# Kernel tuning notes

Measured on AMD Instinct MI355X. Metric: run time of the kernel, lower is better.

Reference implementation:

```python
import jax, jax.numpy as jnp
import numpy as np

B, S, DIM, H, DH = 1, 4096, 2048, 16, 128
EPS = 1e-5


def setup_inputs() -> dict:
    key = jax.random.key(0)
    ks = jax.random.split(key, 16)
    sc = 0.02
    inp = {
        'hidden_states': jax.random.normal(ks[0], (B, S, DIM), jnp.float32),
        'freqs_cos': jax.random.uniform(ks[1], (1, S, 1, DH), jnp.float32),
        'freqs_sin': jax.random.uniform(ks[2], (1, S, 1, DH), jnp.float32),
        'Wq': jax.random.normal(ks[3], (DIM, DIM), jnp.float32) * sc,
        'bq': jax.random.normal(ks[4], (DIM,), jnp.float32) * sc,
        'Wk': jax.random.normal(ks[5], (DIM, DIM), jnp.float32) * sc,
        'bk': jax.random.normal(ks[6], (DIM,), jnp.float32) * sc,
        'Wv': jax.random.normal(ks[7], (DIM, DIM), jnp.float32) * sc,
        'bv': jax.random.normal(ks[8], (DIM,), jnp.float32) * sc,
        'Wo': jax.random.normal(ks[9], (DIM, DIM), jnp.float32) * sc,
        'bo': jax.random.normal(ks[10], (DIM,), jnp.float32) * sc,
        'gq': jnp.ones((DIM,), jnp.float32),
        'gk': jnp.ones((DIM,), jnp.float32),
    }
    return inp


def _rmsnorm(x, g):
    var = jnp.mean(jnp.square(x), axis=-1, keepdims=True)
    return x * jax.lax.rsqrt(var + EPS) * g


def _apply_rope(x, freqs_cos, freqs_sin):
    # x: [B,S,H,DH]; interleaved rotary as in WanAttnProcessor
    x1 = x[..., 0::2]
    x2 = x[..., 1::2]
    cos = freqs_cos[..., 0::2]
    sin = freqs_sin[..., 1::2]
    o1 = x1 * cos - x2 * sin
    o2 = x1 * sin + x2 * cos
    return jnp.stack([o1, o2], axis=-1).reshape(x.shape)


def reference(hidden_states, freqs_cos, freqs_sin, Wq, bq, Wk, bk, Wv, bv, Wo, bo, gq, gk):
    q = hidden_states @ Wq + bq
    k = hidden_states @ Wk + bk
    v = hidden_states @ Wv + bv
    q = _rmsnorm(q, gq)
    k = _rmsnorm(k, gk)
    q = q.reshape(B, S, H, DH)
    k = k.reshape(B, S, H, DH)
    v = v.reshape(B, S, H, DH)
    q = _apply_rope(q, freqs_cos, freqs_sin)
    k = _apply_rope(k, freqs_cos, freqs_sin)
    scale = 1.0 / np.sqrt(DH).astype(np.float32)
    scores = jnp.einsum('bqhd,bkhd->bhqk', q, k) * scale
    attn = jax.nn.softmax(scores, axis=-1)
    out = jnp.einsum('bhqk,bkhd->bqhd', attn, v)
    out = out.reshape(B, S, H * DH)
    return out @ Wo + bo
```

## Files before the change

kernel.cpp:

```cpp
#include <hip/hip_runtime.h>
#include <hip/hip_bf16.h>

#define SEQ 4096
#define DIMC 2048
#define NH 16
#define DHD 128

typedef short s8v __attribute__((ext_vector_type(8)));
typedef float f4v __attribute__((ext_vector_type(4)));
typedef __bf16 bf8 __attribute__((ext_vector_type(8)));
typedef float f4 __attribute__((ext_vector_type(4)));

typedef __attribute__((address_space(3))) void lds_t;
typedef __attribute__((address_space(1))) void gbl_t;

__device__ __attribute__((aligned(256))) short g_h[(size_t)SEQ * DIMC];
__device__ __attribute__((aligned(256))) short g_q[(size_t)SEQ * DIMC];
__device__ __attribute__((aligned(256))) short g_k[(size_t)SEQ * DIMC];
__device__ __attribute__((aligned(256))) short g_v[(size_t)SEQ * DIMC];
__device__ __attribute__((aligned(256))) short g_vt[(size_t)DIMC * SEQ];
__device__ __attribute__((aligned(256))) short g_wt[4][(size_t)DIMC * DIMC];

__device__ __forceinline__ float b2f(short s) {
    union { unsigned u; float f; } v;
    v.u = ((unsigned)(unsigned short)s) << 16;
    return v.f;
}
__device__ __forceinline__ short f2b(float f) {
    union { float f; unsigned u; } v;
    v.f = f;
    unsigned b = v.u;
    b += 0x7FFFu + ((b >> 16) & 1u);
    return (short)(b >> 16);
}
__device__ __forceinline__ f4 mfma16(bf8 a, bf8 b, f4 c) {
    return __builtin_amdgcn_mfma_f32_16x16x32_bf16(a, b, c, 0, 0, 0);
}
__device__ __forceinline__ void gl_lds16(const short* g, short* l) {
    __builtin_amdgcn_global_load_lds((gbl_t*)g, (lds_t*)l, 16, 0, 0);
}

__global__ __launch_bounds__(256) void conv_h(const float* __restrict__ src) {
    size_t i = ((size_t)blockIdx.x * 256 + threadIdx.x) * 8;
    f4v u0 = *reinterpret_cast<const f4v*>(src + i);
    f4v u1 = *reinterpret_cast<const f4v*>(src + i + 4);
    s8v t;
    for (int j = 0; j < 4; ++j) { t[j] = f2b(u0[j]); t[4 + j] = f2b(u1[j]); }
    *reinterpret_cast<s8v*>(g_h + i) = t;
}

__global__ __launch_bounds__(256) void prep_w(const float* __restrict__ W0,
                                              const float* __restrict__ W1,
                                              const float* __restrict__ W2,
                                              const float* __restrict__ W3) {
    __shared__ __attribute__((aligned(16))) float t[64][68];
    const int z = blockIdx.z;
    const float* W = (z == 0) ? W0 : (z == 1) ? W1 : (z == 2) ? W2 : W3;
    short* WT = g_wt[z];
    const int r0 = blockIdx.y * 64, c0 = blockIdx.x * 64;
    const int tid = threadIdx.x;
    for (int i = 0; i < 4; ++i) {
        int slot = tid + i * 256;
        int r = slot >> 4, c4 = (slot & 15) * 4;
        *reinterpret_cast<f4v*>(&t[r][c4]) =
            *reinterpret_cast<const f4v*>(&W[(size_t)(r0 + r) * DIMC + c0 + c4]);
    }
    __syncthreads();
    for (int i = 0; i < 2; ++i) {
        int slot = tid + i * 256;
        int n = slot >> 3, k8 = (slot & 7) * 8;
        s8v o;
        for (int j = 0; j < 8; ++j) o[j] = f2b(t[k8 + j][n]);
        *reinterpret_cast<s8v*>(&WT[(size_t)(c0 + n) * DIMC + r0 + k8]) = o;
    }
}

template <int DSTF>
__device__ __forceinline__ void gemm_body(const short* __restrict__ X,
                                          const short* __restrict__ Bw,
                                          const float* __restrict__ bias,
                                          short* __restrict__ Yb,
                                          float* __restrict__ Yf,
                                          int bm, int bn) {
    __shared__ __attribute__((aligned(16))) short As[128 * 32];
    __shared__ __attribute__((aligned(16))) short Bs[128 * 32];
    const int tid = threadIdx.x;
    const int w = tid >> 6, lane = tid & 63;
    const int l16 = lane & 15, quad = lane >> 4;
    const int wm = w & 1, wn = w >> 1;

    f4 acc[4][4];
    for (int mi = 0; mi < 4; ++mi)
        for (int ni = 0; ni < 4; ++ni) acc[mi][ni] = (f4)0.0f;

    const int s0 = tid, s1 = tid + 256;
    const int ra0 = s0 >> 2, ca0 = (s0 & 3) * 8;
    const int ra1 = s1 >> 2, ca1 = (s1 & 3) * 8;
    const size_t xo0 = (size_t)(bm * 128 + ra0) * DIMC + ca0;
    const size_t xo1 = (size_t)(bm * 128 + ra1) * DIMC + ca1;
    const size_t bo0 = (size_t)(bn * 128 + ra0) * DIMC + ca0;
    const size_t bo1 = (size_t)(bn * 128 + ra1) * DIMC + ca1;
    short* lda0 = As + (size_t)(0 * 256 + w * 64) * 8;
    short* lda1 = As + (size_t)(1 * 256 + w * 64) * 8;
    short* ldb0 = Bs + (size_t)(0 * 256 + w * 64) * 8;
    short* ldb1 = Bs + (size_t)(1 * 256 + w * 64) * 8;

    for (int kb = 0; kb < DIMC; kb += 32) {
        __syncthreads();
        gl_lds16(X + xo0 + kb, lda0);
        gl_lds16(X + xo1 + kb, lda1);
        gl_lds16(Bw + bo0 + kb, ldb0);
        gl_lds16(Bw + bo1 + kb, ldb1);
        __syncthreads();
        bf8 af[4], bfr[4];
        for (int mi = 0; mi < 4; ++mi)
            af[mi] = *reinterpret_cast<const bf8*>(As + (wm * 64 + mi * 16 + l16) * 32 + quad * 8);
        for (int ni = 0; ni < 4; ++ni)
            bfr[ni] = *reinterpret_cast<const bf8*>(Bs + (wn * 64 + ni * 16 + l16) * 32 + quad * 8);
        for (int mi = 0; mi < 4; ++mi)
            for (int ni = 0; ni < 4; ++ni)
                acc[mi][ni] = mfma16(af[mi], bfr[ni], acc[mi][ni]);
    }

    for (int ni = 0; ni < 4; ++ni) {
        int col = bn * 128 + wn * 64 + ni * 16 + l16;
        float bcol = bias[col];
        for (int mi = 0; mi < 4; ++mi) {
            int row = bm * 128 + wm * 64 + mi * 16 + quad * 4;
            for (int r = 0; r < 4; ++r) {
                if (DSTF)
                    Yf[(size_t)(row + r) * DIMC + col] = acc[mi][ni][r] + bcol;
                else
                    Yb[(size_t)(row + r) * DIMC + col] = f2b(acc[mi][ni][r] + bcol);
            }
        }
    }
}

__global__ __launch_bounds__(256, 2) void gemm_qkv(const float* __restrict__ bq,
                                                   const float* __restrict__ bk,
                                                   const float* __restrict__ bv) {
    const int z = blockIdx.z;
    const float* bias = (z == 0) ? bq : (z == 1) ? bk : bv;
    short* Y = (z == 0) ? g_q : (z == 1) ? g_k : g_v;
    gemm_body<0>(g_h, g_wt[z], bias, Y, nullptr, blockIdx.y, blockIdx.x);
}

__global__ __launch_bounds__(256, 2) void gemm_o(const float* __restrict__ bias,
                                                 float* __restrict__ Yf) {
    gemm_body<1>(g_q, g_wt[3], bias, nullptr, Yf, blockIdx.y, blockIdx.x);
}

__global__ __launch_bounds__(256) void rmsnorm_rope(const float* __restrict__ gq,
                                                    const float* __restrict__ gk,
                                                    const float* __restrict__ fc,
                                                    const float* __restrict__ fs) {
    __shared__ float partial[4];
    __shared__ float totsh;
    const int s = blockIdx.x;
    const int which = blockIdx.y;
    short* x = which ? g_k : g_q;
    const float* g = which ? gk : gq;
    const int tid = threadIdx.x;
    const int d0 = tid * 8;

    s8v xv = *reinterpret_cast<const s8v*>(&x[(size_t)s * DIMC + d0]);
    float xf[8];
    float ssq = 0.0f;
    for (int j = 0; j < 8; ++j) { xf[j] = b2f(xv[j]); ssq += xf[j] * xf[j]; }
    for (int off = 32; off; off >>= 1) ssq += __shfl_down(ssq, off);
    if ((tid & 63) == 0) partial[tid >> 6] = ssq;
    __syncthreads();
    if (tid == 0) totsh = partial[0] + partial[1] + partial[2] + partial[3];
    __syncthreads();
    float rs = rsqrtf(totsh * (1.0f / (float)DIMC) + 1e-5f);
    if (which == 0) rs *= 0.12751744f;

    f4v g0 = *reinterpret_cast<const f4v*>(&g[d0]);
    f4v g1 = *reinterpret_cast<const f4v*>(&g[d0 + 4]);
    float xn[8];
    for (int j = 0; j < 4; ++j) { xn[j] = xf[j] * rs * g0[j]; xn[4 + j] = xf[4 + j] * rs * g1[j]; }

    s8v ov;
    for (int p = 0; p < 4; ++p) {
        int e = d0 + 2 * p;
        int hd = e & (DHD - 1);
        float c = fc[(size_t)s * DHD + hd];
        float sn = fs[(size_t)s * DHD + hd + 1];
        float x1 = xn[2 * p], x2 = xn[2 * p + 1];
        ov[2 * p]     = f2b(x1 * c - x2 * sn);
        ov[2 * p + 1] = f2b(x1 * sn + x2 * c);
    }
    *reinterpret_cast<s8v*>(&x[(size_t)s * DIMC + d0]) = ov;
}

__global__ __launch_bounds__(256) void transpose_v() {
    __shared__ __attribute__((aligned(16))) short t[64][72];
    const int h = blockIdx.z, dt = blockIdx.y, st = blockIdx.x;
    const int tid = threadIdx.x;
    const short* src = g_v + (size_t)st * 64 * DIMC + h * DHD + dt * 64;
    for (int i = 0; i < 2; ++i) {
        int slot = tid + i * 256;
        int s = slot >> 3, d8 = (slot & 7) * 8;
        *reinterpret_cast<s8v*>(&t[s][d8]) =
            *reinterpret_cast<const s8v*>(src + (size_t)s * DIMC + d8);
    }
    __syncthreads();
    short* dst = g_vt + (size_t)(h * DHD + dt * 64) * SEQ + st * 64;
    for (int i = 0; i < 2; ++i) {
        int slot = tid + i * 256;
        int d = slot >> 3, s8_ = (slot & 7) * 8;
        s8v o;
        for (int j = 0; j < 8; ++j) o[j] = t[s8_ + j][d];
        *reinterpret_cast<s8v*>(dst + (size_t)d * SEQ + s8_) = o;
    }
}

__global__ __launch_bounds__(256, 2) void attn_k() {
    __shared__ __attribute__((aligned(16))) short Ks0[64 * 128];
    __shared__ __attribute__((aligned(16))) short Vt0[128 * 64];
    __shared__ __attribute__((aligned(16))) __hip_bfloat16 Psb[4][16][72];

    const int h = blockIdx.y;
    const int q0 = blockIdx.x * 128;
    const int tid = threadIdx.x;
    const int w = tid >> 6, lane = tid & 63;
    const int l16 = lane & 15, quad = lane >> 4;

    bf8 qf[2][4];
    for (int qs = 0; qs < 2; ++qs) {
        const short* qb = g_q + (size_t)(q0 + w * 32 + qs * 16 + l16) * DIMC + h * DHD + quad * 8;
        for (int c = 0; c < 4; ++c)
            qf[qs][c] = *reinterpret_cast<const bf8*>(qb + c * 32);
    }
    f4 of[2][8];
    for (int qs = 0; qs < 2; ++qs)
        for (int n = 0; n < 8; ++n) of[qs][n] = (f4)0.0f;
    f4 lacc[2] = {(f4)0.0f, (f4)0.0f};

    s8v ob;
    for (int j = 0; j < 8; ++j) ob[j] = (short)0x3F80;
    const bf8 vones = __builtin_bit_cast(bf8, ob);

    const short* Kbase = g_k + h * DHD;
    const short* Vbase = g_vt + (size_t)h * DHD * SEQ;

    const short* kp[4];
    const short* vp[4];
    for (int i = 0; i < 4; ++i) {
        int s = tid + i * 256;
        int krow = s >> 4, kcb = ((s & 15) - krow) & 15;
        int vd = s >> 3, vkb = ((s & 7) - vd) & 7;
        kp[i] = Kbase + (size_t)krow * DIMC + kcb * 8;
        vp[i] = Vbase + (size_t)vd * SEQ + vkb * 8;
    }

    for (int kt = 0; kt < SEQ; kt += 64) {
        __syncthreads();
        for (int i = 0; i < 4; ++i) {
            gl_lds16(kp[i], Ks0 + (size_t)(i * 256 + w * 64) * 8);
            kp[i] += (size_t)64 * DIMC;
        }
        for (int i = 0; i < 4; ++i) {
            gl_lds16(vp[i], Vt0 + (size_t)(i * 256 + w * 64) * 8);
            vp[i] += 64;
        }
        __syncthreads();

        f4 sa[2][4];
        for (int qs = 0; qs < 2; ++qs)
            for (int ns = 0; ns < 4; ++ns) sa[qs][ns] = (f4)0.0f;
        for (int ns = 0; ns < 4; ++ns)
            for (int c = 0; c < 4; ++c) {
                bf8 kf = *reinterpret_cast<const bf8*>(
                    Ks0 + (ns * 16 + l16) * 128 + ((c * 4 + quad + l16) & 15) * 8);
                sa[0][ns] = mfma16(qf[0][c], kf, sa[0][ns]);
                sa[1][ns] = mfma16(qf[1][c], kf, sa[1][ns]);
            }

        bf8 pa[2][2];
        for (int qs = 0; qs < 2; ++qs) {
            for (int ns = 0; ns < 4; ++ns) {
                float p0 = exp2f(sa[qs][ns][0]);
                float p1 = exp2f(sa[qs][ns][1]);
                float p2 = exp2f(sa[qs][ns][2]);
                float p3 = exp2f(sa[qs][ns][3]);
                __hip_bfloat162 c01 = __float22bfloat162_rn({p0, p1});
                __hip_bfloat162 c23 = __float22bfloat162_rn({p2, p3});
                int col = ns * 16 + l16;
                Psb[w][quad * 4 + 0][col] = c01.x;
                Psb[w][quad * 4 + 1][col] = c01.y;
                Psb[w][quad * 4 + 2][col] = c23.x;
                Psb[w][quad * 4 + 3][col] = c23.y;
            }
            __builtin_amdgcn_s_waitcnt(0);
            for (int c2 = 0; c2 < 2; ++c2)
                pa[qs][c2] = *reinterpret_cast<const bf8*>(&Psb[w][l16][c2 * 32 + quad * 8]);
        }

        lacc[0] = mfma16(pa[0][0], vones, lacc[0]);
        lacc[0] = mfma16(pa[0][1], vones, lacc[0]);
        lacc[1] = mfma16(pa[1][0], vones, lacc[1]);
        lacc[1] = mfma16(pa[1][1], vones, lacc[1]);

        for (int c2 = 0; c2 < 2; ++c2)
            for (int n = 0; n < 8; ++n) {
                bf8 vf = *reinterpret_cast<const bf8*>(
                    Vt0 + (n * 16 + l16) * 64 + ((c2 * 4 + quad + l16) & 7) * 8);
                of[0][n] = mfma16(pa[0][c2], vf, of[0][n]);
                of[1][n] = mfma16(pa[1][c2], vf, of[1][n]);
            }
    }

    for (int qs = 0; qs < 2; ++qs)
        for (int r = 0; r < 4; ++r) {
            float inv = 1.0f / lacc[qs][r];
            int row = q0 + w * 32 + qs * 16 + quad * 4 + r;
            for (int n = 0; n < 8; ++n)
                g_q[(size_t)row * DIMC + h * DHD + n * 16 + l16] = f2b(of[qs][n][r] * inv);
        }
}

extern "C" void kernel_launch(void* const* d_in, const int* in_sizes, int n_in,
                              void* d_out, int out_size, void* d_ws, size_t ws_size,
                              hipStream_t stream) {
    const float* hidden = (const float*)d_in[0];
    const float* fc = (const float*)d_in[1];
    const float* fs = (const float*)d_in[2];
    const float* Wq = (const float*)d_in[3];
    const float* bq = (const float*)d_in[4];
    const float* Wk = (const float*)d_in[5];
    const float* bk = (const float*)d_in[6];
    const float* Wv = (const float*)d_in[7];
    const float* bv = (const float*)d_in[8];
    const float* Wo = (const float*)d_in[9];
    const float* bo = (const float*)d_in[10];
    const float* gq = (const float*)d_in[11];
    const float* gk = (const float*)d_in[12];

    dim3 blk(256);
    conv_h<<<dim3(4096), blk, 0, stream>>>(hidden);
    prep_w<<<dim3(32, 32, 4), blk, 0, stream>>>(Wq, Wk, Wv, Wo);
    gemm_qkv<<<dim3(16, 32, 3), blk, 0, stream>>>(bq, bk, bv);
    rmsnorm_rope<<<dim3(SEQ, 2), blk, 0, stream>>>(gq, gk, fc, fs);
    transpose_v<<<dim3(64, 2, NH), blk, 0, stream>>>();
    attn_k<<<dim3(32, NH), blk, 0, stream>>>();
    gemm_o<<<dim3(16, 32), blk, 0, stream>>>(bo, (float*)d_out);
}
```

Before: 557.0 us.

## Double-buffer K/V tiles in attention with async prefetch and priority hints

Splits the K and V shared-memory tiles into two buffers and prefetches the next tile directly into LDS while the current tile is processed. A partial vmcnt wait keeps the new loads in flight. The change also adds s_setprio around the MFMA sections and narrows the P-tile wait to lgkmcnt only. This is meant to hide global load latency behind matrix work, at the cost of twice the LDS footprint, which may reduce occupancy below the two blocks per CU that the launch bounds target.

```diff
diff --git a/kernel.cpp b/kernel.cpp
--- a/kernel.cpp
+++ b/kernel.cpp
@@ -217,8 +217,8 @@
 }
 
 __global__ __launch_bounds__(256, 2) void attn_k() {
-    __shared__ __attribute__((aligned(16))) short Ks0[64 * 128];
-    __shared__ __attribute__((aligned(16))) short Vt0[128 * 64];
+    __shared__ __attribute__((aligned(16))) short Ks0[2][64 * 128];
+    __shared__ __attribute__((aligned(16))) short Vt0[2][128 * 64];
     __shared__ __attribute__((aligned(16))) __hip_bfloat16 Psb[4][16][72];
 
     const int h = blockIdx.y;
@@ -255,28 +255,50 @@
         vp[i] = Vbase + (size_t)vd * SEQ + vkb * 8;
     }
 
+    for (int i = 0; i < 4; ++i) {
+        gl_lds16(kp[i], &Ks0[0][(size_t)(i * 256 + w * 64) * 8]);
+        kp[i] += (size_t)64 * DIMC;
+    }
+    for (int i = 0; i < 4; ++i) {
+        gl_lds16(vp[i], &Vt0[0][(size_t)(i * 256 + w * 64) * 8]);
+        vp[i] += 64;
+    }
+
     for (int kt = 0; kt < SEQ; kt += 64) {
-        __syncthreads();
-        for (int i = 0; i < 4; ++i) {
-            gl_lds16(kp[i], Ks0 + (size_t)(i * 256 + w * 64) * 8);
-            kp[i] += (size_t)64 * DIMC;
+        const int cur = (kt >> 6) & 1;
+        if (kt + 64 < SEQ) {
+            const int nxt = cur ^ 1;
+            for (int i = 0; i < 4; ++i) {
+                gl_lds16(kp[i], &Ks0[nxt][(size_t)(i * 256 + w * 64) * 8]);
+                kp[i] += (size_t)64 * DIMC;
+            }
+            for (int i = 0; i < 4; ++i) {
+                gl_lds16(vp[i], &Vt0[nxt][(size_t)(i * 256 + w * 64) * 8]);
+                vp[i] += 64;
+            }
+            asm volatile("s_waitcnt vmcnt(8)" ::: "memory");
+        } else {
+            asm volatile("s_waitcnt vmcnt(0)" ::: "memory");
         }
-        for (int i = 0; i < 4; ++i) {
-            gl_lds16(vp[i], Vt0 + (size_t)(i * 256 + w * 64) * 8);
-            vp[i] += 64;
-        }
-        __syncthreads();
+        __builtin_amdgcn_sched_barrier(0);
+        __builtin_amdgcn_s_barrier();
+        __builtin_amdgcn_sched_barrier(0);
+
+        const short* Ks = Ks0[cur];
+        const short* Vt = Vt0[cur];
 
         f4 sa[2][4];
         for (int qs = 0; qs < 2; ++qs)
             for (int ns = 0; ns < 4; ++ns) sa[qs][ns] = (f4)0.0f;
+        __builtin_amdgcn_s_setprio(1);
         for (int ns = 0; ns < 4; ++ns)
             for (int c = 0; c < 4; ++c) {
                 bf8 kf = *reinterpret_cast<const bf8*>(
-                    Ks0 + (ns * 16 + l16) * 128 + ((c * 4 + quad + l16) & 15) * 8);
+                    Ks + (ns * 16 + l16) * 128 + ((c * 4 + quad + l16) & 15) * 8);
                 sa[0][ns] = mfma16(qf[0][c], kf, sa[0][ns]);
                 sa[1][ns] = mfma16(qf[1][c], kf, sa[1][ns]);
             }
+        __builtin_amdgcn_s_setprio(0);
 
         bf8 pa[2][2];
         for (int qs = 0; qs < 2; ++qs) {
@@ -293,11 +315,13 @@
                 Psb[w][quad * 4 + 2][col] = c23.x;
                 Psb[w][quad * 4 + 3][col] = c23.y;
             }
-            __builtin_amdgcn_s_waitcnt(0);
+            asm volatile("s_waitcnt lgkmcnt(0)" ::: "memory");
+            __builtin_amdgcn_sched_barrier(0);
             for (int c2 = 0; c2 < 2; ++c2)
                 pa[qs][c2] = *reinterpret_cast<const bf8*>(&Psb[w][l16][c2 * 32 + quad * 8]);
         }
 
+        __builtin_amdgcn_s_setprio(1);
         lacc[0] = mfma16(pa[0][0], vones, lacc[0]);
         lacc[0] = mfma16(pa[0][1], vones, lacc[0]);
         lacc[1] = mfma16(pa[1][0], vones, lacc[1]);
@@ -306,10 +330,14 @@
         for (int c2 = 0; c2 < 2; ++c2)
             for (int n = 0; n < 8; ++n) {
                 bf8 vf = *reinterpret_cast<const bf8*>(
-                    Vt0 + (n * 16 + l16) * 64 + ((c2 * 4 + quad + l16) & 7) * 8);
+                    Vt + (n * 16 + l16) * 64 + ((c2 * 4 + quad + l16) & 7) * 8);
                 of[0][n] = mfma16(pa[0][c2], vf, of[0][n]);
                 of[1][n] = mfma16(pa[1][c2], vf, of[1][n]);
             }
+        __builtin_amdgcn_s_setprio(0);
+
+        __builtin_amdgcn_s_barrier();
+        __builtin_amdgcn_sched_barrier(0);
     }
 
     for (int qs = 0; qs < 2; ++qs)
```

Result: faster. 540.2 us (-3.0%).
